# Optimization experiments

Measured on AMD Instinct MI355X. Metric: run time of the kernel, lower is better.

The kernel has to match this reference:

```python
import jax, jax.numpy as jnp
import numpy as np

N_NODES = 50000
IN_C = 128
OUT_C = 128
N_EDGES = 800000


def setup_inputs() -> dict:
    key = jax.random.key(0)
    k1, k2, k3, k4, k5 = jax.random.split(key, 5)
    x = jax.random.normal(k1, (N_NODES, IN_C), dtype=jnp.float32)
    edge_index = jax.random.randint(k2, (2, N_EDGES), 0, N_NODES, dtype=jnp.int64)
    s = 1.0 / np.sqrt(IN_C)
    # PyG SAGEConv: lin_l applied to aggregated neighbors (carries bias), lin_r to root (no bias)
    W_l = jax.random.uniform(k3, (OUT_C, IN_C), dtype=jnp.float32, minval=-s, maxval=s)
    b_l = jax.random.uniform(k4, (OUT_C,), dtype=jnp.float32, minval=-s, maxval=s)
    W_r = jax.random.uniform(k5, (OUT_C, IN_C), dtype=jnp.float32, minval=-s, maxval=s)
    return {"x": x, "edge_index": edge_index, "W_l": W_l, "b_l": b_l, "W_r": W_r}


def reference(x, edge_index, W_l, b_l, W_r):
    src = edge_index[0]  # message source j
    dst = edge_index[1]  # target node i
    # gather + scatter-mean aggregation over in-neighbors
    msgs = x[src]  # [E, in_c]
    agg = jax.ops.segment_sum(msgs, dst, num_segments=N_NODES)  # [N, in_c]
    cnt = jax.ops.segment_sum(jnp.ones((N_EDGES,), dtype=x.dtype), dst, num_segments=N_NODES)
    mean = agg / jnp.maximum(cnt, 1.0)[:, None]
    # linear transform: neighbor branch + root branch
    out = mean @ W_l.T + b_l + x @ W_r.T  # [N, out_c]
    # L2 normalize (F.normalize, p=2, eps=1e-12)
    norm = jnp.maximum(jnp.linalg.norm(out, axis=-1, keepdims=True), 1e-12)
    return out / norm
```

## Files before the change

### kernel.cpp

```cpp
#include <hip/hip_runtime.h>
#include <hip/hip_bf16.h>

#define IN_C 128
#define OUT_CH 128
#define NHB 64
#define NB_MAX 800
#define NBW_MAX 200

typedef __attribute__((ext_vector_type(8))) short bf16x8;
typedef __attribute__((ext_vector_type(4))) float f32x4;

__device__ __forceinline__ unsigned pk2(float a, float b) {
    union { __hip_bfloat162 h; unsigned u; } c;
    c.h = __float22bfloat162_rn(make_float2(a, b));
    return c.u;
}
__device__ __forceinline__ float blo(unsigned v) { return __uint_as_float(v << 16); }
__device__ __forceinline__ float bhi(unsigned v) { return __uint_as_float(v & 0xffff0000u); }

__device__ __forceinline__ void add8(float* a, const uint4 v) {
    a[0] += blo(v.x); a[1] += bhi(v.x);
    a[2] += blo(v.y); a[3] += bhi(v.y);
    a[4] += blo(v.z); a[5] += bhi(v.z);
    a[6] += blo(v.w); a[7] += bhi(v.w);
}

__global__ __launch_bounds__(512) void k_hist(
        const float* __restrict__ x, const float* __restrict__ Wl,
        const float* __restrict__ Wr, const int* __restrict__ dst,
        uint* __restrict__ bh, uint* __restrict__ xb,
        unsigned short* __restrict__ Wcat,
        int N, int E, int NBW, int slice, int useXb) {
    __shared__ uint h8[NBW_MAX];
    if (blockIdx.x < NHB) {
        for (int w = threadIdx.x; w < NBW; w += 512) h8[w] = 0u;
        __syncthreads();
        const int lo = blockIdx.x * slice;
        const int hi = min(E, lo + slice);
        for (int e = lo + threadIdx.x; e < hi; e += 512) {
            const int bin = dst[e] >> 6;
            atomicAdd(&h8[bin >> 2], 1u << ((bin & 3) * 8));
        }
        __syncthreads();
        uint* row = bh + (size_t)blockIdx.x * NBW;
        for (int w = threadIdx.x; w < NBW; w += 512) row[w] = h8[w];
    } else {
        const int PB = gridDim.x - NHB;
        const int NX8 = useXb ? (N + 1) * 16 : 0;
        const int TOT = NX8 + 128 * 256;
        const int T = PB * 512;
        for (int idx = (blockIdx.x - NHB) * 512 + threadIdx.x; idx < TOT; idx += T) {
            if (idx < NX8) {
                uint4 o = make_uint4(0u, 0u, 0u, 0u);
                if (idx < N * 16) {
                    const float4* p = reinterpret_cast<const float4*>(x + (size_t)idx * 8);
                    const float4 v0 = p[0], v1 = p[1];
                    o.x = pk2(v0.x, v0.y); o.y = pk2(v0.z, v0.w);
                    o.z = pk2(v1.x, v1.y); o.w = pk2(v1.z, v1.w);
                }
                reinterpret_cast<uint4*>(xb)[idx] = o;
            } else {
                const int w = idx - NX8;
                const int n = w >> 8, k = w & 255;
                const float v = (k < IN_C) ? Wl[n * IN_C + k] : Wr[n * IN_C + (k - IN_C)];
                union { __hip_bfloat16 h2; unsigned short s; } cc;
                cc.h2 = __float2bfloat16(v);
                Wcat[w] = cc.s;
            }
        }
    }
}

__global__ __launch_bounds__(256) void k_scan(
        const uint* __restrict__ bh, unsigned short* __restrict__ bhb,
        int* __restrict__ bincnt, int* __restrict__ binoff, int NB, int NBW) {
    __shared__ uint hst[NHB * NBW_MAX];
    __shared__ int bc[NB_MAX];
    __shared__ int sb[256];
    __shared__ int carry;
    const int t = threadIdx.x;
    for (int i = t; i < NHB * NBW; i += 256) hst[i] = bh[i];
    if (t == 0) carry = 0;
    __syncthreads();
    if (t < NBW) {
        uint r0 = 0, r1 = 0, r2 = 0, r3 = 0;
        const int b0 = 4 * t;
        for (int s = 0; s < NHB; ++s) {
            const uint v = hst[s * NBW + t];
            unsigned short* bb = bhb + (size_t)s * NB;
            if (b0 + 0 < NB) bb[b0 + 0] = (unsigned short)r0;
            if (b0 + 1 < NB) bb[b0 + 1] = (unsigned short)r1;
            if (b0 + 2 < NB) bb[b0 + 2] = (unsigned short)r2;
            if (b0 + 3 < NB) bb[b0 + 3] = (unsigned short)r3;
            r0 += v & 255u;         r1 += (v >> 8) & 255u;
            r2 += (v >> 16) & 255u; r3 += (v >> 24) & 255u;
        }
        if (b0 + 0 < NB) bc[b0 + 0] = (int)r0;
        if (b0 + 1 < NB) bc[b0 + 1] = (int)r1;
        if (b0 + 2 < NB) bc[b0 + 2] = (int)r2;
        if (b0 + 3 < NB) bc[b0 + 3] = (int)r3;
    }
    __syncthreads();
    for (int i = t; i < NB; i += 256) bincnt[i] = bc[i];
    for (int base = 0; base < NB; base += 256) {
        const int idx = base + t;
        const int v = (idx < NB) ? bc[idx] : 0;
        sb[t] = v; __syncthreads();
        for (int d = 1; d < 256; d <<= 1) {
            const int u = (t >= d) ? sb[t - d] : 0;
            __syncthreads();
            sb[t] += u;
            __syncthreads();
        }
        const int inc = sb[t];
        const int c = carry;
        __syncthreads();
        if (idx < NB) binoff[idx] = c + inc - v;
        if (t == 255) carry = c + inc;
        __syncthreads();
    }
}

__global__ __launch_bounds__(512) void k_scatter(
        const int* __restrict__ src, const int* __restrict__ dst,
        const unsigned short* __restrict__ bhb, const int* __restrict__ binoff,
        int* __restrict__ ebinbuf, int NB, int E, int slice) {
    __shared__ int cur[NB_MAX];
    const unsigned short* myb = bhb + (size_t)blockIdx.x * NB;
    for (int b = threadIdx.x; b < NB; b += 512) cur[b] = binoff[b] + (int)myb[b];
    __syncthreads();
    const int lo = blockIdx.x * slice;
    const int hi = min(E, lo + slice);
    for (int e = lo + threadIdx.x; e < hi; e += 512) {
        const int d = dst[e];
        const int pos = atomicAdd(&cur[d >> 6], 1);
        ebinbuf[pos] = src[e] | ((d & 63) << 17);
    }
}

template<bool BF16X>
__global__ __launch_bounds__(256) void k_sage(
        const float* __restrict__ x, const uint* __restrict__ xb,
        const int* __restrict__ ebinbuf, const int* __restrict__ binoff,
        const int* __restrict__ bincnt, const unsigned short* __restrict__ Wcat,
        const float* __restrict__ bl, float* __restrict__ out, int N) {
    __shared__ int elist[1600];
    __shared__ int sorted[560];
    __shared__ int cnt16[16], start16[16], csr16[16];
    __shared__ unsigned short feat[16][264];
    __shared__ float ssh[4][16];

    const int tid  = threadIdx.x;
    const int lane = tid & 63;
    const int wv   = tid >> 6;
    const int g    = lane >> 4;
    const int cl   = lane & 15;
    const int bin  = blockIdx.x >> 2;
    const int q    = blockIdx.x & 3;
    const int node0 = (bin << 6) + (q << 4);
    const int nl   = wv * 4 + g;
    const int node = node0 + nl;

    const int boff = binoff[bin];
    const int bcnt = min(bincnt[bin], 1600);
    for (int i = tid; i < bcnt; i += 256) elist[i] = ebinbuf[boff + i];
    if (tid < 16) cnt16[tid] = 0;
    __syncthreads();
    for (int i = tid; i < bcnt; i += 256) {
        const int dl = elist[i] >> 17;
        if ((dl >> 4) == q) atomicAdd(&cnt16[dl & 15], 1);
    }
    __syncthreads();
    if (tid == 0) {
        int run = 0;
        for (int i = 0; i < 16; ++i) { start16[i] = run; csr16[i] = run; run += cnt16[i]; }
    }
    __syncthreads();
    for (int i = tid; i < bcnt; i += 256) {
        const int v = elist[i];
        const int dl = v >> 17;
        if ((dl >> 4) == q) {
            const int p = atomicAdd(&csr16[dl & 15], 1);
            sorted[p] = v & 0x1FFFF;
        }
    }
    __syncthreads();

    const int m  = (node < N) ? cnt16[nl] : 0;
    const int s0 = start16[nl];

    float a[8];
#pragma unroll
    for (int i = 0; i < 8; ++i) a[i] = 0.f;

    if (BF16X) {
        const uint* rowb = xb + cl * 4;
        for (int j = 0; j < m; j += 4) {
            const int q0 = sorted[s0 + j];
            const int q1 = (j + 1 < m) ? sorted[s0 + j + 1] : N;
            const int q2 = (j + 2 < m) ? sorted[s0 + j + 2] : N;
            const int q3 = (j + 3 < m) ? sorted[s0 + j + 3] : N;
            const uint4 v0 = *reinterpret_cast<const uint4*>(rowb + (size_t)q0 * 64);
            const uint4 v1 = *reinterpret_cast<const uint4*>(rowb + (size_t)q1 * 64);
            const uint4 v2 = *reinterpret_cast<const uint4*>(rowb + (size_t)q2 * 64);
            const uint4 v3 = *reinterpret_cast<const uint4*>(rowb + (size_t)q3 * 64);
            add8(a, v0); add8(a, v1); add8(a, v2); add8(a, v3);
        }
    } else {
        for (int j = 0; j < m; j += 4) {
#pragma unroll
            for (int t = 0; t < 4; ++t) {
                if (j + t < m) {
                    const int qq = sorted[s0 + j + t];
                    const float4* pr = reinterpret_cast<const float4*>(
                        x + (size_t)qq * IN_C + cl * 8);
                    const float4 u0 = pr[0], u1 = pr[1];
                    a[0] += u0.x; a[1] += u0.y; a[2] += u0.z; a[3] += u0.w;
                    a[4] += u1.x; a[5] += u1.y; a[6] += u1.z; a[7] += u1.w;
                }
            }
        }
    }
    const float inv = 1.0f / fmaxf((float)m, 1.0f);
    uint4 pw;
    pw.x = pk2(a[0] * inv, a[1] * inv); pw.y = pk2(a[2] * inv, a[3] * inv);
    pw.z = pk2(a[4] * inv, a[5] * inv); pw.w = pk2(a[6] * inv, a[7] * inv);
    char* frow = reinterpret_cast<char*>(&feat[nl][0]);
    *reinterpret_cast<uint4*>(frow + cl * 16) = pw;

    uint4 xr = make_uint4(0u, 0u, 0u, 0u);
    if (node < N) {
        if (BF16X) {
            xr = *reinterpret_cast<const uint4*>(xb + (size_t)node * 64 + cl * 4);
        } else {
            const float4* pr = reinterpret_cast<const float4*>(
                x + (size_t)node * IN_C + cl * 8);
            const float4 u0 = pr[0], u1 = pr[1];
            xr.x = pk2(u0.x, u0.y); xr.y = pk2(u0.z, u0.w);
            xr.z = pk2(u1.x, u1.y); xr.w = pk2(u1.z, u1.w);
        }
    }
    *reinterpret_cast<uint4*>(frow + 256 + cl * 16) = xr;
    __syncthreads();

    const int m_lane = lane & 15;
    const int kq = lane >> 4;
    f32x4 acc[2] = {{0, 0, 0, 0}, {0, 0, 0, 0}};
    const char* arow  = reinterpret_cast<const char*>(&feat[m_lane][0]) + kq * 16;
    const char* bbase = reinterpret_cast<const char*>(Wcat)
                      + (size_t)(wv * 32 + m_lane) * 512 + kq * 16;
#pragma unroll
    for (int ks = 0; ks < 8; ++ks) {
        const bf16x8 af = *reinterpret_cast<const bf16x8*>(arow + ks * 64);
        const bf16x8 b0 = *reinterpret_cast<const bf16x8*>(bbase + ks * 64);
        const bf16x8 b1 = *reinterpret_cast<const bf16x8*>(bbase + 16 * 512 + ks * 64);
        acc[0] = __builtin_amdgcn_mfma_f32_16x16x32_bf16(af, b0, acc[0], 0, 0, 0);
        acc[1] = __builtin_amdgcn_mfma_f32_16x16x32_bf16(af, b1, acc[1], 0, 0, 0);
    }

    const float bb0 = bl[wv * 32 + m_lane];
    const float bb1 = bl[wv * 32 + 16 + m_lane];
#pragma unroll
    for (int r = 0; r < 4; ++r) { acc[0][r] += bb0; acc[1][r] += bb1; }

#pragma unroll
    for (int r = 0; r < 4; ++r) {
        float v = acc[0][r] * acc[0][r] + acc[1][r] * acc[1][r];
        v += __shfl_xor(v, 1); v += __shfl_xor(v, 2);
        v += __shfl_xor(v, 4); v += __shfl_xor(v, 8);
        if (m_lane == 0) ssh[wv][kq * 4 + r] = v;
    }
    __syncthreads();

#pragma unroll
    for (int r = 0; r < 4; ++r) {
        const int nn = kq * 4 + r;
        const int nd = node0 + nn;
        if (nd < N) {
            const float ss = ssh[0][nn] + ssh[1][nn] + ssh[2][nn] + ssh[3][nn];
            const float rn = 1.0f / fmaxf(sqrtf(ss), 1e-12f);
            out[(size_t)nd * OUT_CH + wv * 32 + m_lane]      = acc[0][r] * rn;
            out[(size_t)nd * OUT_CH + wv * 32 + 16 + m_lane] = acc[1][r] * rn;
        }
    }
}

static inline size_t alignup(size_t v) { return (v + 15) & ~(size_t)15; }

extern "C" void kernel_launch(void* const* d_in, const int* in_sizes, int n_in,
                              void* d_out, int out_size, void* d_ws, size_t ws_size,
                              hipStream_t stream) {
    const float* x    = (const float*)d_in[0];
    const int*   edge = (const int*)d_in[1];
    const float* Wl   = (const float*)d_in[2];
    const float* bl   = (const float*)d_in[3];
    const float* Wr   = (const float*)d_in[4];
    float*       out  = (float*)d_out;

    const int N = in_sizes[0] / IN_C;
    const int E = in_sizes[1] / 2;
    const int* src = edge;
    const int* dst = edge + E;
    const int NB  = (N + 63) / 64;
    const int NBW = (NB + 3) / 4;

    char* p = (char*)d_ws;
    uint* bh      = (uint*)p;            p += alignup((size_t)NHB * NBW * 4);
    unsigned short* bhb = (unsigned short*)p;  p += alignup((size_t)NHB * NB * 2);
    int* bincnt   = (int*)p;             p += alignup(((size_t)NB + 4) * 4);
    int* binoff   = (int*)p;             p += alignup(((size_t)NB + 4) * 4);
    int* ebinbuf  = (int*)p;             p += alignup((size_t)E * 4);
    unsigned short* Wcat = (unsigned short*)p;  p += alignup(128 * 256 * 2);
    uint* xb = (uint*)p;
    const size_t need = (size_t)(p - (char*)d_ws) + ((size_t)N + 1) * IN_C * 2;
    const int useXb = (ws_size >= need) ? 1 : 0;

    const int slice = (E + NHB - 1) / NHB;
    k_hist   <<<NHB + 256, 512, 0, stream>>>(x, Wl, Wr, dst, bh, xb, Wcat,
                                             N, E, NBW, slice, useXb);
    k_scan   <<<1, 256, 0, stream>>>(bh, bhb, bincnt, binoff, NB, NBW);
    k_scatter<<<NHB, 512, 0, stream>>>(src, dst, bhb, binoff, ebinbuf, NB, E, slice);

    const int blocksN = NB * 4;
    if (useXb)
        k_sage<true> <<<blocksN, 256, 0, stream>>>(x, xb, ebinbuf, binoff, bincnt,
                                                   Wcat, bl, out, N);
    else
        k_sage<false><<<blocksN, 256, 0, stream>>>(x, xb, ebinbuf, binoff, bincnt,
                                                   Wcat, bl, out, N);
}
```

Measured before the change: 105.2 us.

## Fuse histogram, scan and scatter into one kernel with fixed-capacity bins

Replaces the three-kernel binning pipeline (per-block histogram, single-block scan, scatter) with one kernel. Each block claims space in a fixed-capacity slot per bin through global atomics on a zeroed counter array, then scatters its edges directly. This removes two launches and the serial single-block scan, and doubles the number of histogram blocks. In exchange it adds a memset and padded bin storage, and edges beyond the per-bin capacity are silently dropped, which only works if in-degree per 64-node bin stays small enough.

```diff
diff --git a/kernel.cpp b/kernel.cpp
--- a/kernel.cpp
+++ b/kernel.cpp
@@ -3,9 +3,11 @@
 
 #define IN_C 128
 #define OUT_CH 128
-#define NHB 64
+#define NHB 128
 #define NB_MAX 800
 #define NBW_MAX 200
+#define CAPSH 11
+#define CAP (1 << CAPSH)
 
 typedef __attribute__((ext_vector_type(8))) short bf16x8;
 typedef __attribute__((ext_vector_type(4))) float f32x4;
@@ -25,13 +27,15 @@
     a[6] += blo(v.w); a[7] += bhi(v.w);
 }
 
-__global__ __launch_bounds__(512) void k_hist(
+__global__ __launch_bounds__(512) void k_build(
         const float* __restrict__ x, const float* __restrict__ Wl,
-        const float* __restrict__ Wr, const int* __restrict__ dst,
-        uint* __restrict__ bh, uint* __restrict__ xb,
+        const float* __restrict__ Wr, const int* __restrict__ src,
+        const int* __restrict__ dst, int* __restrict__ bincur,
+        int* __restrict__ ebinbuf, uint* __restrict__ xb,
         unsigned short* __restrict__ Wcat,
         int N, int E, int NBW, int slice, int useXb) {
     __shared__ uint h8[NBW_MAX];
+    __shared__ int cur[NB_MAX];
     if (blockIdx.x < NHB) {
         for (int w = threadIdx.x; w < NBW; w += 512) h8[w] = 0u;
         __syncthreads();
@@ -42,8 +46,22 @@
             atomicAdd(&h8[bin >> 2], 1u << ((bin & 3) * 8));
         }
         __syncthreads();
-        uint* row = bh + (size_t)blockIdx.x * NBW;
-        for (int w = threadIdx.x; w < NBW; w += 512) row[w] = h8[w];
+        for (int w = threadIdx.x; w < NBW; w += 512) {
+            const uint v = h8[w];
+#pragma unroll
+            for (int i = 0; i < 4; ++i) {
+                const int cnt = (int)((v >> (i * 8)) & 255u);
+                const int b = 4 * w + i;
+                cur[b] = cnt ? atomicAdd(&bincur[b], cnt) : 0;
+            }
+        }
+        __syncthreads();
+        for (int e = lo + threadIdx.x; e < hi; e += 512) {
+            const int d = dst[e];
+            const int bin = d >> 6;
+            const int pos = atomicAdd(&cur[bin], 1);
+            if (pos < CAP) ebinbuf[(bin << CAPSH) + pos] = src[e] | ((d & 63) << 17);
+        }
     } else {
         const int PB = gridDim.x - NHB;
         const int NX8 = useXb ? (N + 1) * 16 : 0;
@@ -71,78 +89,11 @@
     }
 }
 
-__global__ __launch_bounds__(256) void k_scan(
-        const uint* __restrict__ bh, unsigned short* __restrict__ bhb,
-        int* __restrict__ bincnt, int* __restrict__ binoff, int NB, int NBW) {
-    __shared__ uint hst[NHB * NBW_MAX];
-    __shared__ int bc[NB_MAX];
-    __shared__ int sb[256];
-    __shared__ int carry;
-    const int t = threadIdx.x;
-    for (int i = t; i < NHB * NBW; i += 256) hst[i] = bh[i];
-    if (t == 0) carry = 0;
-    __syncthreads();
-    if (t < NBW) {
-        uint r0 = 0, r1 = 0, r2 = 0, r3 = 0;
-        const int b0 = 4 * t;
-        for (int s = 0; s < NHB; ++s) {
-            const uint v = hst[s * NBW + t];
-            unsigned short* bb = bhb + (size_t)s * NB;
-            if (b0 + 0 < NB) bb[b0 + 0] = (unsigned short)r0;
-            if (b0 + 1 < NB) bb[b0 + 1] = (unsigned short)r1;
-            if (b0 + 2 < NB) bb[b0 + 2] = (unsigned short)r2;
-            if (b0 + 3 < NB) bb[b0 + 3] = (unsigned short)r3;
-            r0 += v & 255u;         r1 += (v >> 8) & 255u;
-            r2 += (v >> 16) & 255u; r3 += (v >> 24) & 255u;
-        }
-        if (b0 + 0 < NB) bc[b0 + 0] = (int)r0;
-        if (b0 + 1 < NB) bc[b0 + 1] = (int)r1;
-        if (b0 + 2 < NB) bc[b0 + 2] = (int)r2;
-        if (b0 + 3 < NB) bc[b0 + 3] = (int)r3;
-    }
-    __syncthreads();
-    for (int i = t; i < NB; i += 256) bincnt[i] = bc[i];
-    for (int base = 0; base < NB; base += 256) {
-        const int idx = base + t;
-        const int v = (idx < NB) ? bc[idx] : 0;
-        sb[t] = v; __syncthreads();
-        for (int d = 1; d < 256; d <<= 1) {
-            const int u = (t >= d) ? sb[t - d] : 0;
-            __syncthreads();
-            sb[t] += u;
-            __syncthreads();
-        }
-        const int inc = sb[t];
-        const int c = carry;
-        __syncthreads();
-        if (idx < NB) binoff[idx] = c + inc - v;
-        if (t == 255) carry = c + inc;
-        __syncthreads();
-    }
-}
-
-__global__ __launch_bounds__(512) void k_scatter(
-        const int* __restrict__ src, const int* __restrict__ dst,
-        const unsigned short* __restrict__ bhb, const int* __restrict__ binoff,
-        int* __restrict__ ebinbuf, int NB, int E, int slice) {
-    __shared__ int cur[NB_MAX];
-    const unsigned short* myb = bhb + (size_t)blockIdx.x * NB;
-    for (int b = threadIdx.x; b < NB; b += 512) cur[b] = binoff[b] + (int)myb[b];
-    __syncthreads();
-    const int lo = blockIdx.x * slice;
-    const int hi = min(E, lo + slice);
-    for (int e = lo + threadIdx.x; e < hi; e += 512) {
-        const int d = dst[e];
-        const int pos = atomicAdd(&cur[d >> 6], 1);
-        ebinbuf[pos] = src[e] | ((d & 63) << 17);
-    }
-}
-
 template<bool BF16X>
 __global__ __launch_bounds__(256) void k_sage(
         const float* __restrict__ x, const uint* __restrict__ xb,
-        const int* __restrict__ ebinbuf, const int* __restrict__ binoff,
-        const int* __restrict__ bincnt, const unsigned short* __restrict__ Wcat,
+        const int* __restrict__ ebinbuf, const int* __restrict__ bincur,
+        const unsigned short* __restrict__ Wcat,
         const float* __restrict__ bl, float* __restrict__ out, int N) {
     __shared__ int elist[1600];
     __shared__ int sorted[560];
@@ -161,8 +112,8 @@
     const int nl   = wv * 4 + g;
     const int node = node0 + nl;
 
-    const int boff = binoff[bin];
-    const int bcnt = min(bincnt[bin], 1600);
+    const int boff = bin << CAPSH;
+    const int bcnt = min(min(bincur[bin], CAP), 1600);
     for (int i = tid; i < bcnt; i += 256) elist[i] = ebinbuf[boff + i];
     if (tid < 16) cnt16[tid] = 0;
     __syncthreads();
@@ -305,27 +256,24 @@
     const int NBW = (NB + 3) / 4;
 
     char* p = (char*)d_ws;
-    uint* bh      = (uint*)p;            p += alignup((size_t)NHB * NBW * 4);
-    unsigned short* bhb = (unsigned short*)p;  p += alignup((size_t)NHB * NB * 2);
-    int* bincnt   = (int*)p;             p += alignup(((size_t)NB + 4) * 4);
-    int* binoff   = (int*)p;             p += alignup(((size_t)NB + 4) * 4);
-    int* ebinbuf  = (int*)p;             p += alignup((size_t)E * 4);
+    int* bincur  = (int*)p;              p += alignup(((size_t)NB + 4) * 4);
+    int* ebinbuf = (int*)p;              p += alignup((size_t)NB * CAP * 4);
     unsigned short* Wcat = (unsigned short*)p;  p += alignup(128 * 256 * 2);
     uint* xb = (uint*)p;
     const size_t need = (size_t)(p - (char*)d_ws) + ((size_t)N + 1) * IN_C * 2;
     const int useXb = (ws_size >= need) ? 1 : 0;
 
+    hipMemsetAsync(bincur, 0, ((size_t)NB + 4) * 4, stream);
+
     const int slice = (E + NHB - 1) / NHB;
-    k_hist   <<<NHB + 256, 512, 0, stream>>>(x, Wl, Wr, dst, bh, xb, Wcat,
-                                             N, E, NBW, slice, useXb);
-    k_scan   <<<1, 256, 0, stream>>>(bh, bhb, bincnt, binoff, NB, NBW);
-    k_scatter<<<NHB, 512, 0, stream>>>(src, dst, bhb, binoff, ebinbuf, NB, E, slice);
+    k_build<<<NHB + 256, 512, 0, stream>>>(x, Wl, Wr, src, dst, bincur, ebinbuf,
+                                           xb, Wcat, N, E, NBW, slice, useXb);
 
     const int blocksN = NB * 4;
     if (useXb)
-        k_sage<true> <<<blocksN, 256, 0, stream>>>(x, xb, ebinbuf, binoff, bincnt,
+        k_sage<true> <<<blocksN, 256, 0, stream>>>(x, xb, ebinbuf, bincur,
                                                    Wcat, bl, out, N);
     else
-        k_sage<false><<<blocksN, 256, 0, stream>>>(x, xb, ebinbuf, binoff, bincnt,
+        k_sage<false><<<blocksN, 256, 0, stream>>>(x, xb, ebinbuf, bincur,
                                                    Wcat, bl, out, N);
 }
```

Result: faster. 94.88 us (-9.8%).
